# Performance work log

Hardware: AMD Instinct MI355X
Metric: run time of the kernel (lower is better)

The kernel has to match this reference:

```python
import jax, jax.numpy as jnp
import numpy as np

B, NE, DE = 4096, 64, 96
NA, NACT = 8, 16
DH, NH, OD = 256, 4, 64
HD = DH // NH


def setup_inputs() -> dict:
    key = jax.random.key(0)
    ks = jax.random.split(key, 16)
    s = 0.02
    entities = jax.random.normal(ks[0], (B, NE, DE), jnp.float32)
    entity_mask = jax.random.randint(ks[1], (B, NE), 0, 2, jnp.int32)
    obs_mask = jax.random.randint(ks[2], (B, NE, NE), 0, 2, jnp.int32)
    act_ids = jax.random.randint(ks[3], (B, NA), 0, NACT)
    actions_onehot = jax.nn.one_hot(act_ids, NACT, dtype=jnp.float32)
    return {
        "entities": entities,
        "entity_mask": entity_mask,
        "obs_mask": obs_mask,
        "actions_onehot": actions_onehot,
        "We": jax.random.normal(ks[4], (DE, DH), jnp.float32) * s,
        "be": jnp.zeros((DH,), jnp.float32),
        "Wa": jax.random.normal(ks[5], (NACT, DH), jnp.float32) * s,
        "Win": jax.random.normal(ks[6], (DH, 3 * DH), jnp.float32) * s,
        "Wout": jax.random.normal(ks[7], (DH, DH), jnp.float32) * s,
        "bout": jnp.zeros((DH,), jnp.float32),
        "Wm1": jax.random.normal(ks[8], (DH, DH), jnp.float32) * s,
        "bm1": jnp.zeros((DH,), jnp.float32),
        "Wm2": jax.random.normal(ks[9], (DH, OD), jnp.float32) * s,
        "bm2": jnp.zeros((OD,), jnp.float32),
        "Wl1": jax.random.normal(ks[10], (DH, DH), jnp.float32) * s,
        "bl1": jnp.zeros((DH,), jnp.float32),
        "Wl2": jax.random.normal(ks[11], (DH, OD), jnp.float32) * s,
        "bl2": jnp.zeros((OD,), jnp.float32),
    }


def reference(entities, entity_mask, obs_mask, actions_onehot,
              We, be, Wa, Win, Wout, bout,
              Wm1, bm1, Wm2, bm2, Wl1, bl1, Wl2, bl2):
    # entity encode + action embed, scattered into first NA entity slots
    he = entities @ We + be                      # [B, NE, DH]
    ha = actions_onehot @ Wa                     # [B, NA, DH]
    ha_pad = jnp.zeros_like(he).at[:, :NA].set(ha)
    x = jax.nn.relu(he + ha_pad)                 # [B, NE, DH]

    # multi-head attention: NA agent queries attend to NE entities
    qkv = x @ Win                                # [B, NE, 3*DH]
    q, k, v = jnp.split(qkv, 3, axis=-1)
    q = q[:, :NA].reshape(B, NA, NH, HD)
    k = k.reshape(B, NE, NH, HD)
    v = v.reshape(B, NE, NH, HD)
    logits = jnp.einsum('bqhd,bkhd->bhqk', q, k) / jnp.sqrt(jnp.float32(HD))
    pre = obs_mask[:, :NA, :NE].astype(bool)[:, None, :, :]  # [B,1,NA,NE]
    logits = jnp.where(pre, -jnp.inf, logits)
    w = jax.nn.softmax(logits, axis=-1)
    w = jnp.where(jnp.isnan(w), 0.0, w)          # fully-masked rows -> 0
    attn = jnp.einsum('bhqk,bkhd->bqhd', w, v).reshape(B, NA, DH)
    attn = attn @ Wout + bout
    post = entity_mask[:, :NA].astype(bool)[..., None]  # [B, NA, 1]
    hidden = jax.nn.relu(jnp.where(post, 0.0, attn))

    mean = jax.nn.relu(hidden @ Wm1 + bm1) @ Wm2 + bm2
    logvar = jnp.clip(jax.nn.relu(hidden @ Wl1 + bl1) @ Wl2 + bl2, -10.0, 0.0)
    return mean, logvar
```

## Files before the change

kernel.cpp:

```cpp
#include <hip/hip_runtime.h>
#include <hip/hip_bf16.h>
#include <math.h>

typedef __attribute__((ext_vector_type(8))) short short8;
typedef __attribute__((ext_vector_type(4))) float f32x4;

#define DEVINL static __device__ __forceinline__

static constexpr int NBPB = 2;
static constexpr int NBLK = 4096 / NBPB;

static constexpr int WE_OFF  = 0;
static constexpr int WQ_OFF  = 24576;
static constexpr int WK_OFF  = 90112;
static constexpr int WV_OFF  = 155648;
static constexpr int WO_OFF  = 221184;
static constexpr int WM1_OFF = 286720;
static constexpr int WM2_OFF = 352256;
static constexpr int WL1_OFF = 368640;
static constexpr int WL2_OFF = 434176;

static constexpr int XOFF    = 0;
static constexpr int KOFF    = 65536;
static constexpr int VOFF    = 65536;
static constexpr int HID_OFF = 65536;
static constexpr int M1_OFF  = 81920;
static constexpr int L1_OFF  = 98304;
static constexpr int QOFF    = 131072;
static constexpr int WOFF2   = 147456;
static constexpr int EOFF    = 131072;
static constexpr int ACT_OFF = 155648;
static constexpr int LDS_BYTES = 155712;

DEVINL unsigned short f2bf(float f) {
  union { float f; unsigned u; } x; x.f = f;
  unsigned r = x.u + 0x7fffu + ((x.u >> 16) & 1u);
  return (unsigned short)(r >> 16);
}

DEVINL f32x4 mfma(short8 a, short8 b, f32x4 c) {
  return __builtin_amdgcn_mfma_f32_16x16x32_bf16(a, b, c, 0, 0, 0);
}

DEVINL short8 ldfrag(const unsigned short* wf, int off, int nt, int kt, int nkt, int lane) {
  return *(const short8*)(wf + off + ((nt * nkt + kt) << 9) + (lane << 3));
}

DEVINL short8 lda512(const char* sm, int base, int row, int colbyte) {
  return *(const short8*)(sm + base + row * 512 + (colbyte ^ ((row & 7) << 4)));
}

DEVINL void stb512(char* sm, int base, int row, int col, float v) {
  *(unsigned short*)(sm + base + row * 512 + ((col * 2) ^ ((row & 7) << 4))) = f2bf(v);
}

__global__ __launch_bounds__(512) void prep_kernel(
    const float* We, const float* Win, const float* Wout, const float* Wm1,
    const float* Wm2, const float* Wl1, const float* Wl2, unsigned short* wf) {
  const int m = blockIdx.y;
  const int Ks[9]   = {96, 256, 256, 256, 256, 256, 256, 256, 256};
  const int Ns[9]   = {256, 256, 256, 256, 256, 256, 64, 256, 64};
  const int lds_[9] = {256, 768, 768, 768, 256, 256, 64, 256, 64};
  const int coff[9] = {0, 0, 256, 512, 0, 0, 0, 0, 0};
  const int dsto[9] = {WE_OFF, WQ_OFF, WK_OFF, WV_OFF, WO_OFF, WM1_OFF, WM2_OFF, WL1_OFF, WL2_OFF};
  const float* srcs[9] = {We, Win, Win, Win, Wout, Wm1, Wm2, Wl1, Wl2};
  const int K = Ks[m], N = Ns[m], nkt = K / 32;
  const int total = (N / 16) * nkt * 512;
  const int idx = blockIdx.x * 512 + threadIdx.x;
  if (idx >= total) return;
  const int j = idx & 7, lane = (idx >> 3) & 63;
  const int kt = (idx >> 9) % nkt, nt = idx / (512 * nkt);
  const int row = kt * 32 + ((lane >> 4) << 3) + j;
  const int col = nt * 16 + (lane & 15);
  wf[dsto[m] + idx] = f2bf(srcs[m][(long)row * lds_[m] + coff[m] + col]);
}

__global__ __launch_bounds__(512, 2) void fused_kernel(
    const float* __restrict__ entities, const int* __restrict__ entity_mask,
    const int* __restrict__ obs_mask, const float* __restrict__ acts,
    const float* __restrict__ Wa, const float* __restrict__ be,
    const float* __restrict__ bout, const float* __restrict__ bm1,
    const float* __restrict__ bm2, const float* __restrict__ bl1,
    const float* __restrict__ bl2, const unsigned short* __restrict__ wf,
    float* __restrict__ out) {
  extern __shared__ char sm[];
  const int tid = threadIdx.x;
  const int w = tid >> 6, lane = tid & 63;
  const int g = lane >> 4, c = lane & 15;
  const int ig0 = blockIdx.x * 2;
  const int nt0 = w * 2;

  {
    const int it = tid >> 8, i = tid & 255;
    const int row = i >> 2, q4 = i & 3;
    const float* src = entities + (long)(ig0 + it) * 6144 + row * 96 + q4 * 24;
    const int ebase = EOFF + it * 12288 + row * 192;
    const int sw = (row & 3) << 4;
#pragma unroll
    for (int ch = 0; ch < 3; ++ch) {
      short8 s;
#pragma unroll
      for (int k = 0; k < 8; ++k) s[k] = (short)f2bf(src[ch * 8 + k]);
      *(short8*)(sm + ebase + ((q4 * 48 + ch * 16) ^ sw)) = s;
    }
    if (tid < 16) {
      const float* oh = acts + ((long)(ig0 + (tid >> 3)) * 8 + (tid & 7)) * 16;
      int id = 0;
      for (int a = 0; a < 16; ++a) if (oh[a] > 0.5f) id = a;
      ((int*)(sm + ACT_OFF))[tid] = id;
    }
  }
  __syncthreads();

  {
    f32x4 acc[2][4][2] = {};
#pragma unroll
    for (int kt = 0; kt < 3; ++kt) {
      short8 b0 = ldfrag(wf, WE_OFF, nt0, kt, 3, lane);
      short8 b1 = ldfrag(wf, WE_OFF, nt0 + 1, kt, 3, lane);
#pragma unroll
      for (int it = 0; it < 2; ++it)
#pragma unroll
        for (int mt = 0; mt < 4; ++mt) {
          const int row = mt * 16 + c;
          short8 a = *(const short8*)(sm + EOFF + it * 12288 + row * 192 +
                                      ((kt * 64 + (g << 4)) ^ ((row & 3) << 4)));
          acc[it][mt][0] = mfma(a, b0, acc[it][mt][0]);
          acc[it][mt][1] = mfma(a, b1, acc[it][mt][1]);
        }
    }
    float bev[2] = {be[nt0 * 16 + c], be[nt0 * 16 + 16 + c]};
#pragma unroll
    for (int it = 0; it < 2; ++it)
#pragma unroll
      for (int mt = 0; mt < 4; ++mt)
#pragma unroll
        for (int n = 0; n < 2; ++n)
#pragma unroll
          for (int r = 0; r < 4; ++r) {
            const int row = mt * 16 + g * 4 + r;
            const int col = (nt0 + n) * 16 + c;
            float v = acc[it][mt][n][r] + bev[n];
            if (row < 8) {
              int id = ((const int*)(sm + ACT_OFF))[it * 8 + row];
              v += Wa[id * 256 + col];
            }
            v = fmaxf(v, 0.f);
            stb512(sm, XOFF + it * 32768, row, col, v);
          }
  }
  __syncthreads();

  {
    f32x4 qa[2][2] = {};
#pragma unroll
    for (int kt = 0; kt < 8; ++kt) {
      short8 b0 = ldfrag(wf, WQ_OFF, nt0, kt, 8, lane);
      short8 b1 = ldfrag(wf, WQ_OFF, nt0 + 1, kt, 8, lane);
#pragma unroll
      for (int it = 0; it < 2; ++it) {
        short8 a = lda512(sm, XOFF + it * 32768, c, kt * 64 + (g << 4));
        qa[it][0] = mfma(a, b0, qa[it][0]);
        qa[it][1] = mfma(a, b1, qa[it][1]);
      }
    }
#pragma unroll
    for (int it = 0; it < 2; ++it)
#pragma unroll
      for (int n = 0; n < 2; ++n)
#pragma unroll
        for (int r = 0; r < 4; ++r)
          stb512(sm, QOFF + it * 8192, g * 4 + r, (nt0 + n) * 16 + c, qa[it][n][r]);
  }
  __syncthreads();

  {
    f32x4 acc[2][4][2] = {};
#pragma unroll
    for (int kt = 0; kt < 8; ++kt) {
      short8 b0 = ldfrag(wf, WK_OFF, nt0, kt, 8, lane);
      short8 b1 = ldfrag(wf, WK_OFF, nt0 + 1, kt, 8, lane);
#pragma unroll
      for (int it = 0; it < 2; ++it)
#pragma unroll
        for (int mt = 0; mt < 4; ++mt) {
          short8 a = lda512(sm, XOFF + it * 32768, mt * 16 + c, kt * 64 + (g << 4));
          acc[it][mt][0] = mfma(a, b0, acc[it][mt][0]);
          acc[it][mt][1] = mfma(a, b1, acc[it][mt][1]);
        }
    }
#pragma unroll
    for (int it = 0; it < 2; ++it)
#pragma unroll
      for (int mt = 0; mt < 4; ++mt)
#pragma unroll
        for (int n = 0; n < 2; ++n)
#pragma unroll
          for (int r = 0; r < 4; ++r)
            stb512(sm, KOFF + it * 32768, mt * 16 + g * 4 + r, (nt0 + n) * 16 + c,
                   acc[it][mt][n][r]);
  }
  __syncthreads();

  {
    const int it = w >> 2, h = w & 3;
    const long ig = ig0 + it;
    f32x4 lac[4] = {};
#pragma unroll
    for (int kt = 0; kt < 2; ++kt) {
      const int colb = h * 128 + kt * 64 + (g << 4);
      short8 aq = lda512(sm, QOFF + it * 8192, c, colb);
#pragma unroll
      for (int nt = 0; nt < 4; ++nt) {
        short8 bk = lda512(sm, KOFF + it * 32768, nt * 16 + c, colb);
        lac[nt] = mfma(aq, bk, lac[nt]);
      }
    }
    const int* obs = obs_mask + ig * 4096;
#pragma unroll
    for (int r = 0; r < 4; ++r) {
      const int qi = g * 4 + r;
      float vals[4];
#pragma unroll
      for (int nt = 0; nt < 4; ++nt) {
        int msk = obs[qi * 64 + nt * 16 + c];
        vals[nt] = msk ? -INFINITY : lac[nt][r] * 0.125f;
      }
      float mx = fmaxf(fmaxf(vals[0], vals[1]), fmaxf(vals[2], vals[3]));
#pragma unroll
      for (int d = 1; d < 16; d <<= 1) mx = fmaxf(mx, __shfl_xor(mx, d, 64));
      float s = 0.f;
#pragma unroll
      for (int nt = 0; nt < 4; ++nt) {
        float e = (mx == -INFINITY) ? 0.f : expf(vals[nt] - mx);
        vals[nt] = e; s += e;
      }
#pragma unroll
      for (int d = 1; d < 16; d <<= 1) s += __shfl_xor(s, d, 64);
      const float inv = (s > 0.f) ? 1.f / s : 0.f;
      if (qi < 8) {
#pragma unroll
        for (int nt = 0; nt < 4; ++nt) {
          const int key = nt * 16 + c;
          *(unsigned short*)(sm + WOFF2 + ((it * 4 + h) * 8 + qi) * 128 +
                             ((key * 2) ^ (qi << 4))) = f2bf(vals[nt] * inv);
        }
      }
    }
  }
  __syncthreads();

  {
    f32x4 acc[2][4][2] = {};
#pragma unroll
    for (int kt = 0; kt < 8; ++kt) {
      short8 b0 = ldfrag(wf, WV_OFF, nt0, kt, 8, lane);
      short8 b1 = ldfrag(wf, WV_OFF, nt0 + 1, kt, 8, lane);
#pragma unroll
      for (int it = 0; it < 2; ++it)
#pragma unroll
        for (int mt = 0; mt < 4; ++mt) {
          short8 a = lda512(sm, XOFF + it * 32768, mt * 16 + c, kt * 64 + (g << 4));
          acc[it][mt][0] = mfma(a, b0, acc[it][mt][0]);
          acc[it][mt][1] = mfma(a, b1, acc[it][mt][1]);
        }
    }
#pragma unroll
    for (int it = 0; it < 2; ++it)
#pragma unroll
      for (int mt = 0; mt < 4; ++mt)
#pragma unroll
        for (int n = 0; n < 2; ++n) {
          const int d = (nt0 + n) * 16 + c;
          const int key0 = mt * 16 + g * 4;
          unsigned long long pk = 0;
#pragma unroll
          for (int r = 0; r < 4; ++r)
            pk |= (unsigned long long)f2bf(acc[it][mt][n][r]) << (16 * r);
          *(unsigned long long*)(sm + VOFF + it * 32768 + d * 128 +
                                 ((key0 * 2) ^ ((d & 7) << 4))) = pk;
        }
  }
  __syncthreads();

  {
    const int it = w >> 2, h = w & 3;
    f32x4 aac[4] = {};
#pragma unroll
    for (int kt = 0; kt < 2; ++kt) {
      const int kb = kt * 64 + (g << 4);
      const int wrow = c & 7;
      short8 aw = *(const short8*)(sm + WOFF2 + ((it * 4 + h) * 8 + wrow) * 128 +
                                   (kb ^ (wrow << 4)));
#pragma unroll
      for (int n = 0; n < 4; ++n) {
        const int d = (h * 4 + n) * 16 + c;
        short8 bv = *(const short8*)(sm + VOFF + it * 32768 + d * 128 +
                                     (kb ^ ((d & 7) << 4)));
        aac[n] = mfma(aw, bv, aac[n]);
      }
    }
#pragma unroll
    for (int n = 0; n < 4; ++n)
#pragma unroll
      for (int r = 0; r < 4; ++r)
        stb512(sm, QOFF + it * 8192, g * 4 + r, (h * 4 + n) * 16 + c, aac[n][r]);
  }
  __syncthreads();

  {
    f32x4 acc[2][2] = {};
#pragma unroll
    for (int kt = 0; kt < 8; ++kt) {
      short8 b0 = ldfrag(wf, WO_OFF, nt0, kt, 8, lane);
      short8 b1 = ldfrag(wf, WO_OFF, nt0 + 1, kt, 8, lane);
#pragma unroll
      for (int it = 0; it < 2; ++it) {
        short8 a = lda512(sm, QOFF + it * 8192, c, kt * 64 + (g << 4));
        acc[it][0] = mfma(a, b0, acc[it][0]);
        acc[it][1] = mfma(a, b1, acc[it][1]);
      }
    }
    float bo[2] = {bout[nt0 * 16 + c], bout[nt0 * 16 + 16 + c]};
#pragma unroll
    for (int it = 0; it < 2; ++it) {
      const int* em = entity_mask + (long)(ig0 + it) * 64;
#pragma unroll
      for (int n = 0; n < 2; ++n)
#pragma unroll
        for (int r = 0; r < 4; ++r) {
          const int row = g * 4 + r;
          float v = acc[it][n][r] + bo[n];
          v = em[row] ? 0.f : fmaxf(v, 0.f);
          stb512(sm, HID_OFF + it * 8192, row, (nt0 + n) * 16 + c, v);
        }
    }
  }
  __syncthreads();

  {
    f32x4 am[2][2] = {}, al[2][2] = {};
#pragma unroll
    for (int kt = 0; kt < 8; ++kt) {
      short8 bm0 = ldfrag(wf, WM1_OFF, nt0, kt, 8, lane);
      short8 bm1f = ldfrag(wf, WM1_OFF, nt0 + 1, kt, 8, lane);
      short8 bl0 = ldfrag(wf, WL1_OFF, nt0, kt, 8, lane);
      short8 bl1f = ldfrag(wf, WL1_OFF, nt0 + 1, kt, 8, lane);
#pragma unroll
      for (int it = 0; it < 2; ++it) {
        short8 a = lda512(sm, HID_OFF + it * 8192, c, kt * 64 + (g << 4));
        am[it][0] = mfma(a, bm0, am[it][0]);
        am[it][1] = mfma(a, bm1f, am[it][1]);
        al[it][0] = mfma(a, bl0, al[it][0]);
        al[it][1] = mfma(a, bl1f, al[it][1]);
      }
    }
    float bmv[2] = {bm1[nt0 * 16 + c], bm1[nt0 * 16 + 16 + c]};
    float blv[2] = {bl1[nt0 * 16 + c], bl1[nt0 * 16 + 16 + c]};
#pragma unroll
    for (int it = 0; it < 2; ++it)
#pragma unroll
      for (int n = 0; n < 2; ++n)
#pragma unroll
        for (int r = 0; r < 4; ++r) {
          const int row = g * 4 + r, col = (nt0 + n) * 16 + c;
          stb512(sm, M1_OFF + it * 8192, row, col, fmaxf(am[it][n][r] + bmv[n], 0.f));
          stb512(sm, L1_OFF + it * 8192, row, col, fmaxf(al[it][n][r] + blv[n], 0.f));
        }
  }
  __syncthreads();

  {
    const int isv = (w >= 4);
    const int nt = w & 3;
    const int SRC = (isv ? L1_OFF : M1_OFF);
    const int WOF = (isv ? WL2_OFF : WM2_OFF);
    const float* bias = isv ? bl2 : bm2;
    f32x4 acc[2] = {};
#pragma unroll
    for (int kt = 0; kt < 8; ++kt) {
      short8 b = ldfrag(wf, WOF, nt, kt, 8, lane);
#pragma unroll
      for (int it = 0; it < 2; ++it) {
        short8 a = lda512(sm, SRC + it * 8192, c, kt * 64 + (g << 4));
        acc[it] = mfma(a, b, acc[it]);
      }
    }
    const float bv = bias[nt * 16 + c];
    const long obase = isv ? 2097152L : 0L;
#pragma unroll
    for (int it = 0; it < 2; ++it)
#pragma unroll
      for (int r = 0; r < 4; ++r) {
        const int qi = g * 4 + r;
        if (qi < 8) {
          float v = acc[it][r] + bv;
          if (isv) v = fminf(fmaxf(v, -10.f), 0.f);
          out[obase + (long)(ig0 + it) * 512 + qi * 64 + nt * 16 + c] = v;
        }
      }
  }
}

extern "C" void kernel_launch(void* const* d_in, const int* in_sizes, int n_in,
                              void* d_out, int out_size, void* d_ws, size_t ws_size,
                              hipStream_t stream) {
  const float* entities   = (const float*)d_in[0];
  const int*   entity_mask= (const int*)d_in[1];
  const int*   obs_mask   = (const int*)d_in[2];
  const float* acts       = (const float*)d_in[3];
  const float* We   = (const float*)d_in[4];
  const float* be   = (const float*)d_in[5];
  const float* Wa   = (const float*)d_in[6];
  const float* Win  = (const float*)d_in[7];
  const float* Wout = (const float*)d_in[8];
  const float* bout = (const float*)d_in[9];
  const float* Wm1  = (const float*)d_in[10];
  const float* bm1  = (const float*)d_in[11];
  const float* Wm2  = (const float*)d_in[12];
  const float* bm2  = (const float*)d_in[13];
  const float* Wl1  = (const float*)d_in[14];
  const float* bl1  = (const float*)d_in[15];
  const float* Wl2  = (const float*)d_in[16];
  const float* bl2  = (const float*)d_in[17];
  unsigned short* wf = (unsigned short*)d_ws;

  prep_kernel<<<dim3(128, 9), 512, 0, stream>>>(We, Win, Wout, Wm1, Wm2, Wl1, Wl2, wf);

  hipFuncSetAttribute((const void*)fused_kernel,
                      hipFuncAttributeMaxDynamicSharedMemorySize, LDS_BYTES);
  fused_kernel<<<NBLK, 512, LDS_BYTES, stream>>>(
      entities, entity_mask, obs_mask, acts, Wa, be, bout, bm1, bm2, bl1, bl2,
      wf, (float*)d_out);
}
```

Before: 419.5 us.

## Reassociate attention to skip full K and V projections, use 1024 threads

The attention is rewritten algebraically. Queries are multiplied by the transposed per-head Wk, so logits are computed directly against x and the full K projection is never formed. The softmax weights are applied to x before projecting through Wv, so only 16 query rows are projected instead of 64 entity rows. The block grows to 1024 threads (16 waves) with a new LDS layout that also keeps a transposed copy of x. Entity loading is vectorized, and the prep kernel is rewritten, with a special transposed layout for Wk. Extra barriers and more LDS (164KB) may limit occupancy to one block per CU.

```diff
diff --git a/kernel.cpp b/kernel.cpp
--- a/kernel.cpp
+++ b/kernel.cpp
@@ -4,15 +4,15 @@
 
 typedef __attribute__((ext_vector_type(8))) short short8;
 typedef __attribute__((ext_vector_type(4))) float f32x4;
+typedef __attribute__((ext_vector_type(2))) unsigned int uint2v;
 
 #define DEVINL static __device__ __forceinline__
 
-static constexpr int NBPB = 2;
-static constexpr int NBLK = 4096 / NBPB;
+static constexpr int NBLK = 2048;
 
 static constexpr int WE_OFF  = 0;
 static constexpr int WQ_OFF  = 24576;
-static constexpr int WK_OFF  = 90112;
+static constexpr int WKT_OFF = 90112;
 static constexpr int WV_OFF  = 155648;
 static constexpr int WO_OFF  = 221184;
 static constexpr int WM1_OFF = 286720;
@@ -20,17 +20,19 @@
 static constexpr int WL1_OFF = 368640;
 static constexpr int WL2_OFF = 434176;
 
-static constexpr int XOFF    = 0;
-static constexpr int KOFF    = 65536;
-static constexpr int VOFF    = 65536;
-static constexpr int HID_OFF = 65536;
-static constexpr int M1_OFF  = 81920;
-static constexpr int L1_OFF  = 98304;
-static constexpr int QOFF    = 131072;
-static constexpr int WOFF2   = 147456;
-static constexpr int EOFF    = 131072;
-static constexpr int ACT_OFF = 155648;
-static constexpr int LDS_BYTES = 155712;
+static constexpr int XOFF   = 0;
+static constexpr int WLOFF  = 0;
+static constexpr int ATOFF  = 8192;
+static constexpr int HOFF   = 16384;
+static constexpr int M1OFF  = 24576;
+static constexpr int L1OFF  = 32768;
+static constexpr int XTOFF  = 65536;
+static constexpr int EOFF   = 131072;
+static constexpr int TOFF   = 131072;
+static constexpr int WXOFF  = 131072;
+static constexpr int ACTOFF = 155648;
+static constexpr int QOFF   = 155648;
+static constexpr int LDS_BYTES = 163840;
 
 DEVINL unsigned short f2bf(float f) {
   union { float f; unsigned u; } x; x.f = f;
@@ -46,36 +48,36 @@
   return *(const short8*)(wf + off + ((nt * nkt + kt) << 9) + (lane << 3));
 }
 
-DEVINL short8 lda512(const char* sm, int base, int row, int colbyte) {
-  return *(const short8*)(sm + base + row * 512 + (colbyte ^ ((row & 7) << 4)));
-}
-
-DEVINL void stb512(char* sm, int base, int row, int col, float v) {
-  *(unsigned short*)(sm + base + row * 512 + ((col * 2) ^ ((row & 7) << 4))) = f2bf(v);
-}
-
 __global__ __launch_bounds__(512) void prep_kernel(
     const float* We, const float* Win, const float* Wout, const float* Wm1,
     const float* Wm2, const float* Wl1, const float* Wl2, unsigned short* wf) {
   const int m = blockIdx.y;
-  const int Ks[9]   = {96, 256, 256, 256, 256, 256, 256, 256, 256};
-  const int Ns[9]   = {256, 256, 256, 256, 256, 256, 64, 256, 64};
-  const int lds_[9] = {256, 768, 768, 768, 256, 256, 64, 256, 64};
-  const int coff[9] = {0, 0, 256, 512, 0, 0, 0, 0, 0};
-  const int dsto[9] = {WE_OFF, WQ_OFF, WK_OFF, WV_OFF, WO_OFF, WM1_OFF, WM2_OFF, WL1_OFF, WL2_OFF};
-  const float* srcs[9] = {We, Win, Win, Win, Wout, Wm1, Wm2, Wl1, Wl2};
-  const int K = Ks[m], N = Ns[m], nkt = K / 32;
-  const int total = (N / 16) * nkt * 512;
   const int idx = blockIdx.x * 512 + threadIdx.x;
-  if (idx >= total) return;
-  const int j = idx & 7, lane = (idx >> 3) & 63;
-  const int kt = (idx >> 9) % nkt, nt = idx / (512 * nkt);
-  const int row = kt * 32 + ((lane >> 4) << 3) + j;
-  const int col = nt * 16 + (lane & 15);
-  wf[dsto[m] + idx] = f2bf(srcs[m][(long)row * lds_[m] + coff[m] + col]);
-}
-
-__global__ __launch_bounds__(512, 2) void fused_kernel(
+  if (m == 2) {
+    if (idx >= 65536) return;
+    const int h = idx >> 14, d = (idx >> 6) & 255, hd = idx & 63;
+    const float v = Win[(long)d * 768 + 256 + h * 64 + hd];
+    const int kt = hd >> 5, gg = (hd >> 3) & 3, j = hd & 7;
+    wf[WKT_OFF + (((h * 16 + (d >> 4)) * 2 + kt) << 9) + (gg * 16 + (d & 15)) * 8 + j] =
+        f2bf(v);
+    return;
+  }
+  const int Ks[9]  = {96, 256, 0, 256, 256, 256, 256, 256, 256};
+  const int Ns[9]  = {256, 256, 0, 256, 256, 256, 64, 256, 64};
+  const int ld_[9] = {256, 768, 0, 768, 256, 256, 64, 256, 64};
+  const int co_[9] = {0, 0, 0, 512, 0, 0, 0, 0, 0};
+  const int off[9] = {WE_OFF, WQ_OFF, 0, WV_OFF, WO_OFF, WM1_OFF, WM2_OFF, WL1_OFF, WL2_OFF};
+  const float* S[9] = {We, Win, Win, Win, Wout, Wm1, Wm2, Wl1, Wl2};
+  const int K = Ks[m], N = Ns[m];
+  if (idx >= K * N) return;
+  const int row = idx / N, col = idx - row * N;
+  const float v = S[m][(long)row * ld_[m] + co_[m] + col];
+  const int nkt = K >> 5;
+  wf[off[m] + ((((col >> 4) * nkt) + (row >> 5)) << 9) +
+     ((((row >> 3) & 3) << 4) + (col & 15)) * 8 + (row & 7)] = f2bf(v);
+}
+
+__global__ __launch_bounds__(1024, 4) void fused_kernel(
     const float* __restrict__ entities, const int* __restrict__ entity_mask,
     const int* __restrict__ obs_mask, const float* __restrict__ acts,
     const float* __restrict__ Wa, const float* __restrict__ be,
@@ -88,327 +90,312 @@
   const int w = tid >> 6, lane = tid & 63;
   const int g = lane >> 4, c = lane & 15;
   const int ig0 = blockIdx.x * 2;
-  const int nt0 = w * 2;
-
-  {
-    const int it = tid >> 8, i = tid & 255;
-    const int row = i >> 2, q4 = i & 3;
-    const float* src = entities + (long)(ig0 + it) * 6144 + row * 96 + q4 * 24;
+
+  {
+    const int it = tid >> 9, i = tid & 511;
+    const int row = i >> 3, seg = i & 7;
+    const float* src = entities + (long)(ig0 + it) * 6144 + row * 96 + seg * 12;
     const int ebase = EOFF + it * 12288 + row * 192;
     const int sw = (row & 3) << 4;
 #pragma unroll
-    for (int ch = 0; ch < 3; ++ch) {
-      short8 s;
-#pragma unroll
-      for (int k = 0; k < 8; ++k) s[k] = (short)f2bf(src[ch * 8 + k]);
-      *(short8*)(sm + ebase + ((q4 * 48 + ch * 16) ^ sw)) = s;
+    for (int p = 0; p < 3; ++p) {
+      float4 f = *(const float4*)(src + p * 4);
+      uint2v u;
+      u.x = f2bf(f.x) | ((unsigned)f2bf(f.y) << 16);
+      u.y = f2bf(f.z) | ((unsigned)f2bf(f.w) << 16);
+      *(uint2v*)(sm + ebase + ((seg * 24 + p * 8) ^ sw)) = u;
     }
     if (tid < 16) {
       const float* oh = acts + ((long)(ig0 + (tid >> 3)) * 8 + (tid & 7)) * 16;
       int id = 0;
+#pragma unroll
       for (int a = 0; a < 16; ++a) if (oh[a] > 0.5f) id = a;
-      ((int*)(sm + ACT_OFF))[tid] = id;
-    }
-  }
-  __syncthreads();
-
-  {
-    f32x4 acc[2][4][2] = {};
+      ((int*)(sm + ACTOFF))[tid] = id;
+    }
+  }
+  __syncthreads();
+
+  {
+    f32x4 acc[2][4] = {};
 #pragma unroll
     for (int kt = 0; kt < 3; ++kt) {
-      short8 b0 = ldfrag(wf, WE_OFF, nt0, kt, 3, lane);
-      short8 b1 = ldfrag(wf, WE_OFF, nt0 + 1, kt, 3, lane);
+      short8 b = ldfrag(wf, WE_OFF, w, kt, 3, lane);
 #pragma unroll
       for (int it = 0; it < 2; ++it)
 #pragma unroll
         for (int mt = 0; mt < 4; ++mt) {
           const int row = mt * 16 + c;
           short8 a = *(const short8*)(sm + EOFF + it * 12288 + row * 192 +
-                                      ((kt * 64 + (g << 4)) ^ ((row & 3) << 4)));
-          acc[it][mt][0] = mfma(a, b0, acc[it][mt][0]);
-          acc[it][mt][1] = mfma(a, b1, acc[it][mt][1]);
-        }
-    }
-    float bev[2] = {be[nt0 * 16 + c], be[nt0 * 16 + 16 + c]};
+                                      ((kt * 64 + g * 16) ^ ((row & 3) << 4)));
+          acc[it][mt] = mfma(a, b, acc[it][mt]);
+        }
+    }
+    const int col = w * 16 + c;
+    const float bev = be[col];
 #pragma unroll
     for (int it = 0; it < 2; ++it)
 #pragma unroll
-      for (int mt = 0; mt < 4; ++mt)
-#pragma unroll
-        for (int n = 0; n < 2; ++n)
-#pragma unroll
-          for (int r = 0; r < 4; ++r) {
-            const int row = mt * 16 + g * 4 + r;
-            const int col = (nt0 + n) * 16 + c;
-            float v = acc[it][mt][n][r] + bev[n];
-            if (row < 8) {
-              int id = ((const int*)(sm + ACT_OFF))[it * 8 + row];
-              v += Wa[id * 256 + col];
-            }
-            v = fmaxf(v, 0.f);
-            stb512(sm, XOFF + it * 32768, row, col, v);
+      for (int mt = 0; mt < 4; ++mt) {
+        float vv[4];
+#pragma unroll
+        for (int r = 0; r < 4; ++r) {
+          const int row = mt * 16 + g * 4 + r;
+          float v = acc[it][mt][r] + bev;
+          if (row < 8) {
+            int id = ((const int*)(sm + ACTOFF))[it * 8 + row];
+            v += Wa[id * 256 + col];
           }
-  }
-  __syncthreads();
-
-  {
-    f32x4 qa[2][2] = {};
+          v = fmaxf(v, 0.f);
+          vv[r] = v;
+          *(unsigned short*)(sm + XOFF + it * 32768 + row * 512 +
+                             ((col * 2) ^ ((row & 7) << 4))) = f2bf(v);
+        }
+        uint2v u;
+        u.x = f2bf(vv[0]) | ((unsigned)f2bf(vv[1]) << 16);
+        u.y = f2bf(vv[2]) | ((unsigned)f2bf(vv[3]) << 16);
+        *(uint2v*)(sm + XTOFF + it * 32768 + col * 128 +
+                   ((mt * 32 + g * 8) ^ ((col & 7) << 4))) = u;
+      }
+  }
+  __syncthreads();
+
+  {
+    f32x4 qa = {0.f, 0.f, 0.f, 0.f};
 #pragma unroll
     for (int kt = 0; kt < 8; ++kt) {
-      short8 b0 = ldfrag(wf, WQ_OFF, nt0, kt, 8, lane);
-      short8 b1 = ldfrag(wf, WQ_OFF, nt0 + 1, kt, 8, lane);
-#pragma unroll
-      for (int it = 0; it < 2; ++it) {
-        short8 a = lda512(sm, XOFF + it * 32768, c, kt * 64 + (g << 4));
-        qa[it][0] = mfma(a, b0, qa[it][0]);
-        qa[it][1] = mfma(a, b1, qa[it][1]);
-      }
-    }
-#pragma unroll
-    for (int it = 0; it < 2; ++it)
-#pragma unroll
-      for (int n = 0; n < 2; ++n)
-#pragma unroll
-        for (int r = 0; r < 4; ++r)
-          stb512(sm, QOFF + it * 8192, g * 4 + r, (nt0 + n) * 16 + c, qa[it][n][r]);
-  }
-  __syncthreads();
-
-  {
-    f32x4 acc[2][4][2] = {};
-#pragma unroll
-    for (int kt = 0; kt < 8; ++kt) {
-      short8 b0 = ldfrag(wf, WK_OFF, nt0, kt, 8, lane);
-      short8 b1 = ldfrag(wf, WK_OFF, nt0 + 1, kt, 8, lane);
-#pragma unroll
-      for (int it = 0; it < 2; ++it)
-#pragma unroll
-        for (int mt = 0; mt < 4; ++mt) {
-          short8 a = lda512(sm, XOFF + it * 32768, mt * 16 + c, kt * 64 + (g << 4));
-          acc[it][mt][0] = mfma(a, b0, acc[it][mt][0]);
-          acc[it][mt][1] = mfma(a, b1, acc[it][mt][1]);
-        }
-    }
-#pragma unroll
-    for (int it = 0; it < 2; ++it)
-#pragma unroll
-      for (int mt = 0; mt < 4; ++mt)
-#pragma unroll
-        for (int n = 0; n < 2; ++n)
-#pragma unroll
-          for (int r = 0; r < 4; ++r)
-            stb512(sm, KOFF + it * 32768, mt * 16 + g * 4 + r, (nt0 + n) * 16 + c,
-                   acc[it][mt][n][r]);
-  }
-  __syncthreads();
-
-  {
-    const int it = w >> 2, h = w & 3;
-    const long ig = ig0 + it;
+      short8 b = ldfrag(wf, WQ_OFF, w, kt, 8, lane);
+      short8 a = *(const short8*)(sm + XOFF + (c >> 3) * 32768 + (c & 7) * 512 +
+                                  ((kt * 64 + g * 16) ^ ((c & 7) << 4)));
+      qa = mfma(a, b, qa);
+    }
+#pragma unroll
+    for (int r = 0; r < 4; ++r) {
+      const int qq = g * 4 + r;
+      *(unsigned short*)(sm + QOFF + qq * 512 +
+                         (((w * 16 + c) * 2) ^ ((qq & 7) << 4))) = f2bf(qa[r]);
+    }
+  }
+  __syncthreads();
+
+  {
+    const int h = w >> 2, dq = w & 3;
+    f32x4 ta[4] = {};
+#pragma unroll
+    for (int kt = 0; kt < 2; ++kt) {
+      short8 a = *(const short8*)(sm + QOFF + c * 512 +
+                                  ((h * 128 + kt * 64 + g * 16) ^ ((c & 7) << 4)));
+#pragma unroll
+      for (int n = 0; n < 4; ++n) {
+        short8 b = ldfrag(wf, WKT_OFF, h * 16 + dq * 4 + n, kt, 2, lane);
+        ta[n] = mfma(a, b, ta[n]);
+      }
+    }
+    __syncthreads();
+#pragma unroll
+    for (int n = 0; n < 4; ++n)
+#pragma unroll
+      for (int r = 0; r < 4; ++r) {
+        const int qq = g * 4 + r;
+        const int col = (dq * 4 + n) * 16 + c;
+        *(unsigned short*)(sm + TOFF + h * 8192 + qq * 512 +
+                           ((col * 2) ^ ((qq & 7) << 4))) = f2bf(ta[n][r]);
+      }
+  }
+  __syncthreads();
+
+  {
+    const int it = (w >> 2) & 1, h = w & 3;
+    float wvals[4][4];
     f32x4 lac[4] = {};
-#pragma unroll
-    for (int kt = 0; kt < 2; ++kt) {
-      const int colb = h * 128 + kt * 64 + (g << 4);
-      short8 aq = lda512(sm, QOFF + it * 8192, c, colb);
-#pragma unroll
-      for (int nt = 0; nt < 4; ++nt) {
-        short8 bk = lda512(sm, KOFF + it * 32768, nt * 16 + c, colb);
-        lac[nt] = mfma(aq, bk, lac[nt]);
-      }
-    }
-    const int* obs = obs_mask + ig * 4096;
-#pragma unroll
-    for (int r = 0; r < 4; ++r) {
-      const int qi = g * 4 + r;
-      float vals[4];
-#pragma unroll
-      for (int nt = 0; nt < 4; ++nt) {
-        int msk = obs[qi * 64 + nt * 16 + c];
-        vals[nt] = msk ? -INFINITY : lac[nt][r] * 0.125f;
-      }
-      float mx = fmaxf(fmaxf(vals[0], vals[1]), fmaxf(vals[2], vals[3]));
-#pragma unroll
-      for (int d = 1; d < 16; d <<= 1) mx = fmaxf(mx, __shfl_xor(mx, d, 64));
-      float s = 0.f;
-#pragma unroll
-      for (int nt = 0; nt < 4; ++nt) {
-        float e = (mx == -INFINITY) ? 0.f : expf(vals[nt] - mx);
-        vals[nt] = e; s += e;
-      }
-#pragma unroll
-      for (int d = 1; d < 16; d <<= 1) s += __shfl_xor(s, d, 64);
-      const float inv = (s > 0.f) ? 1.f / s : 0.f;
-      if (qi < 8) {
+    if (w < 8) {
+#pragma unroll
+      for (int kt = 0; kt < 8; ++kt) {
+        short8 a = *(const short8*)(sm + TOFF + h * 8192 + (it * 8 + (c & 7)) * 512 +
+                                    ((kt * 64 + g * 16) ^ ((c & 7) << 4)));
 #pragma unroll
         for (int nt = 0; nt < 4; ++nt) {
           const int key = nt * 16 + c;
-          *(unsigned short*)(sm + WOFF2 + ((it * 4 + h) * 8 + qi) * 128 +
-                             ((key * 2) ^ (qi << 4))) = f2bf(vals[nt] * inv);
-        }
-      }
-    }
-  }
-  __syncthreads();
-
-  {
-    f32x4 acc[2][4][2] = {};
-#pragma unroll
-    for (int kt = 0; kt < 8; ++kt) {
-      short8 b0 = ldfrag(wf, WV_OFF, nt0, kt, 8, lane);
-      short8 b1 = ldfrag(wf, WV_OFF, nt0 + 1, kt, 8, lane);
-#pragma unroll
-      for (int it = 0; it < 2; ++it)
-#pragma unroll
-        for (int mt = 0; mt < 4; ++mt) {
-          short8 a = lda512(sm, XOFF + it * 32768, mt * 16 + c, kt * 64 + (g << 4));
-          acc[it][mt][0] = mfma(a, b0, acc[it][mt][0]);
-          acc[it][mt][1] = mfma(a, b1, acc[it][mt][1]);
-        }
-    }
-#pragma unroll
-    for (int it = 0; it < 2; ++it)
-#pragma unroll
-      for (int mt = 0; mt < 4; ++mt)
-#pragma unroll
-        for (int n = 0; n < 2; ++n) {
-          const int d = (nt0 + n) * 16 + c;
-          const int key0 = mt * 16 + g * 4;
-          unsigned long long pk = 0;
-#pragma unroll
-          for (int r = 0; r < 4; ++r)
-            pk |= (unsigned long long)f2bf(acc[it][mt][n][r]) << (16 * r);
-          *(unsigned long long*)(sm + VOFF + it * 32768 + d * 128 +
-                                 ((key0 * 2) ^ ((d & 7) << 4))) = pk;
-        }
-  }
-  __syncthreads();
-
-  {
-    const int it = w >> 2, h = w & 3;
-    f32x4 aac[4] = {};
-#pragma unroll
-    for (int kt = 0; kt < 2; ++kt) {
-      const int kb = kt * 64 + (g << 4);
-      const int wrow = c & 7;
-      short8 aw = *(const short8*)(sm + WOFF2 + ((it * 4 + h) * 8 + wrow) * 128 +
-                                   (kb ^ (wrow << 4)));
-#pragma unroll
-      for (int n = 0; n < 4; ++n) {
-        const int d = (h * 4 + n) * 16 + c;
-        short8 bv = *(const short8*)(sm + VOFF + it * 32768 + d * 128 +
-                                     (kb ^ ((d & 7) << 4)));
-        aac[n] = mfma(aw, bv, aac[n]);
-      }
-    }
-#pragma unroll
-    for (int n = 0; n < 4; ++n)
-#pragma unroll
-      for (int r = 0; r < 4; ++r)
-        stb512(sm, QOFF + it * 8192, g * 4 + r, (h * 4 + n) * 16 + c, aac[n][r]);
-  }
-  __syncthreads();
-
-  {
-    f32x4 acc[2][2] = {};
-#pragma unroll
-    for (int kt = 0; kt < 8; ++kt) {
-      short8 b0 = ldfrag(wf, WO_OFF, nt0, kt, 8, lane);
-      short8 b1 = ldfrag(wf, WO_OFF, nt0 + 1, kt, 8, lane);
-#pragma unroll
-      for (int it = 0; it < 2; ++it) {
-        short8 a = lda512(sm, QOFF + it * 8192, c, kt * 64 + (g << 4));
-        acc[it][0] = mfma(a, b0, acc[it][0]);
-        acc[it][1] = mfma(a, b1, acc[it][1]);
-      }
-    }
-    float bo[2] = {bout[nt0 * 16 + c], bout[nt0 * 16 + 16 + c]};
-#pragma unroll
-    for (int it = 0; it < 2; ++it) {
-      const int* em = entity_mask + (long)(ig0 + it) * 64;
-#pragma unroll
-      for (int n = 0; n < 2; ++n)
+          short8 b = *(const short8*)(sm + XOFF + it * 32768 + key * 512 +
+                                      ((kt * 64 + g * 16) ^ ((key & 7) << 4)));
+          lac[nt] = mfma(a, b, lac[nt]);
+        }
+      }
+      if (g < 2) {
+        const int* obs = obs_mask + (long)(ig0 + it) * 4096;
 #pragma unroll
         for (int r = 0; r < 4; ++r) {
-          const int row = g * 4 + r;
-          float v = acc[it][n][r] + bo[n];
-          v = em[row] ? 0.f : fmaxf(v, 0.f);
-          stb512(sm, HID_OFF + it * 8192, row, (nt0 + n) * 16 + c, v);
-        }
-    }
-  }
-  __syncthreads();
-
-  {
-    f32x4 am[2][2] = {}, al[2][2] = {};
-#pragma unroll
-    for (int kt = 0; kt < 8; ++kt) {
-      short8 bm0 = ldfrag(wf, WM1_OFF, nt0, kt, 8, lane);
-      short8 bm1f = ldfrag(wf, WM1_OFF, nt0 + 1, kt, 8, lane);
-      short8 bl0 = ldfrag(wf, WL1_OFF, nt0, kt, 8, lane);
-      short8 bl1f = ldfrag(wf, WL1_OFF, nt0 + 1, kt, 8, lane);
-#pragma unroll
-      for (int it = 0; it < 2; ++it) {
-        short8 a = lda512(sm, HID_OFF + it * 8192, c, kt * 64 + (g << 4));
-        am[it][0] = mfma(a, bm0, am[it][0]);
-        am[it][1] = mfma(a, bm1f, am[it][1]);
-        al[it][0] = mfma(a, bl0, al[it][0]);
-        al[it][1] = mfma(a, bl1f, al[it][1]);
-      }
-    }
-    float bmv[2] = {bm1[nt0 * 16 + c], bm1[nt0 * 16 + 16 + c]};
-    float blv[2] = {bl1[nt0 * 16 + c], bl1[nt0 * 16 + 16 + c]};
-#pragma unroll
-    for (int it = 0; it < 2; ++it)
-#pragma unroll
-      for (int n = 0; n < 2; ++n)
-#pragma unroll
-        for (int r = 0; r < 4; ++r) {
-          const int row = g * 4 + r, col = (nt0 + n) * 16 + c;
-          stb512(sm, M1_OFF + it * 8192, row, col, fmaxf(am[it][n][r] + bmv[n], 0.f));
-          stb512(sm, L1_OFF + it * 8192, row, col, fmaxf(al[it][n][r] + blv[n], 0.f));
-        }
-  }
-  __syncthreads();
-
-  {
-    const int isv = (w >= 4);
-    const int nt = w & 3;
-    const int SRC = (isv ? L1_OFF : M1_OFF);
-    const int WOF = (isv ? WL2_OFF : WM2_OFF);
-    const float* bias = isv ? bl2 : bm2;
-    f32x4 acc[2] = {};
-#pragma unroll
-    for (int kt = 0; kt < 8; ++kt) {
-      short8 b = ldfrag(wf, WOF, nt, kt, 8, lane);
-#pragma unroll
-      for (int it = 0; it < 2; ++it) {
-        short8 a = lda512(sm, SRC + it * 8192, c, kt * 64 + (g << 4));
-        acc[it] = mfma(a, b, acc[it]);
-      }
-    }
-    const float bv = bias[nt * 16 + c];
-    const long obase = isv ? 2097152L : 0L;
-#pragma unroll
-    for (int it = 0; it < 2; ++it)
+          const int qi = g * 4 + r;
+          float vals[4];
+#pragma unroll
+          for (int nt = 0; nt < 4; ++nt) {
+            int msk = obs[qi * 64 + nt * 16 + c];
+            vals[nt] = msk ? -INFINITY : lac[nt][r] * 0.125f;
+          }
+          float mx = fmaxf(fmaxf(vals[0], vals[1]), fmaxf(vals[2], vals[3]));
+#pragma unroll
+          for (int d = 1; d < 16; d <<= 1) mx = fmaxf(mx, __shfl_xor(mx, d, 64));
+          float s = 0.f;
+#pragma unroll
+          for (int nt = 0; nt < 4; ++nt) {
+            float e = (mx == -INFINITY) ? 0.f : expf(vals[nt] - mx);
+            vals[nt] = e; s += e;
+          }
+#pragma unroll
+          for (int d = 1; d < 16; d <<= 1) s += __shfl_xor(s, d, 64);
+          const float inv = (s > 0.f) ? 1.f / s : 0.f;
+#pragma unroll
+          for (int nt = 0; nt < 4; ++nt) wvals[r][nt] = vals[nt] * inv;
+        }
+      }
+    }
+    __syncthreads();
+    if (w < 8 && g < 2) {
 #pragma unroll
       for (int r = 0; r < 4; ++r) {
         const int qi = g * 4 + r;
-        if (qi < 8) {
-          float v = acc[it][r] + bv;
-          if (isv) v = fminf(fmaxf(v, -10.f), 0.f);
-          out[obase + (long)(ig0 + it) * 512 + qi * 64 + nt * 16 + c] = v;
-        }
-      }
+#pragma unroll
+        for (int nt = 0; nt < 4; ++nt) {
+          const int key = nt * 16 + c;
+          *(unsigned short*)(sm + WLOFF + ((it * 4 + h) * 8 + qi) * 128 +
+                             ((key * 2) ^ ((qi & 7) << 4))) = f2bf(wvals[r][nt]);
+        }
+      }
+    }
+  }
+  __syncthreads();
+
+  {
+    const int it = w >> 3, h = (w >> 1) & 3, dh = w & 1;
+    f32x4 xa[8] = {};
+#pragma unroll
+    for (int kt = 0; kt < 2; ++kt) {
+      short8 a = *(const short8*)(sm + WLOFF + ((it * 4 + h) * 8 + (c & 7)) * 128 +
+                                  ((kt * 64 + g * 16) ^ ((c & 7) << 4)));
+#pragma unroll
+      for (int n = 0; n < 8; ++n) {
+        const int d = dh * 128 + n * 16 + c;
+        short8 b = *(const short8*)(sm + XTOFF + it * 32768 + d * 128 +
+                                    ((kt * 64 + g * 16) ^ ((d & 7) << 4)));
+        xa[n] = mfma(a, b, xa[n]);
+      }
+    }
+    if (g < 2) {
+#pragma unroll
+      for (int n = 0; n < 8; ++n)
+#pragma unroll
+        for (int r = 0; r < 4; ++r) {
+          const int qq = it * 8 + g * 4 + r;
+          const int col = h * 256 + dh * 128 + n * 16 + c;
+          *(unsigned short*)(sm + WXOFF + qq * 2048 +
+                             ((col * 2) ^ ((qq & 7) << 4))) = f2bf(xa[n][r]);
+        }
+    }
+  }
+  __syncthreads();
+
+  {
+    const int h = w >> 2, n = w & 3;
+    f32x4 aac = {0.f, 0.f, 0.f, 0.f};
+#pragma unroll
+    for (int kt = 0; kt < 8; ++kt) {
+      short8 a = *(const short8*)(sm + WXOFF + c * 2048 +
+                                  ((h * 512 + kt * 64 + g * 16) ^ ((c & 7) << 4)));
+      short8 b = ldfrag(wf, WV_OFF, h * 4 + n, kt, 8, lane);
+      aac = mfma(a, b, aac);
+    }
+#pragma unroll
+    for (int r = 0; r < 4; ++r) {
+      const int qq = g * 4 + r;
+      const int col = (h * 4 + n) * 16 + c;
+      *(unsigned short*)(sm + ATOFF + qq * 512 +
+                         ((col * 2) ^ ((qq & 7) << 4))) = f2bf(aac[r]);
+    }
+  }
+  __syncthreads();
+
+  {
+    f32x4 hc = {0.f, 0.f, 0.f, 0.f};
+#pragma unroll
+    for (int kt = 0; kt < 8; ++kt) {
+      short8 a = *(const short8*)(sm + ATOFF + c * 512 +
+                                  ((kt * 64 + g * 16) ^ ((c & 7) << 4)));
+      short8 b = ldfrag(wf, WO_OFF, w, kt, 8, lane);
+      hc = mfma(a, b, hc);
+    }
+    const int col = w * 16 + c;
+    const float bo = bout[col];
+#pragma unroll
+    for (int r = 0; r < 4; ++r) {
+      const int qq = g * 4 + r;
+      const int em = entity_mask[(long)(ig0 + (qq >> 3)) * 64 + (qq & 7)];
+      float v = hc[r] + bo;
+      v = em ? 0.f : fmaxf(v, 0.f);
+      *(unsigned short*)(sm + HOFF + qq * 512 + ((col * 2) ^ ((qq & 7) << 4))) = f2bf(v);
+    }
+  }
+  __syncthreads();
+
+  {
+    const int which = w >> 3, np = w & 7;
+    const int woff = which ? WL1_OFF : WM1_OFF;
+    const float* bias = which ? bl1 : bm1;
+    const int base = which ? L1OFF : M1OFF;
+    f32x4 mc[2] = {};
+#pragma unroll
+    for (int kt = 0; kt < 8; ++kt) {
+      short8 a = *(const short8*)(sm + HOFF + c * 512 +
+                                  ((kt * 64 + g * 16) ^ ((c & 7) << 4)));
+      short8 b0 = ldfrag(wf, woff, np * 2, kt, 8, lane);
+      short8 b1 = ldfrag(wf, woff, np * 2 + 1, kt, 8, lane);
+      mc[0] = mfma(a, b0, mc[0]);
+      mc[1] = mfma(a, b1, mc[1]);
+    }
+#pragma unroll
+    for (int n = 0; n < 2; ++n) {
+      const int col = (np * 2 + n) * 16 + c;
+      const float bv = bias[col];
+#pragma unroll
+      for (int r = 0; r < 4; ++r) {
+        const int qq = g * 4 + r;
+        float v = fmaxf(mc[n][r] + bv, 0.f);
+        *(unsigned short*)(sm + base + qq * 512 + ((col * 2) ^ ((qq & 7) << 4))) = f2bf(v);
+      }
+    }
+  }
+  __syncthreads();
+
+  if (w < 8) {
+    const int which = w >> 2, nt = w & 3;
+    const int woff = which ? WL2_OFF : WM2_OFF;
+    const int base = which ? L1OFF : M1OFF;
+    const float* bias = which ? bl2 : bm2;
+    f32x4 oc = {0.f, 0.f, 0.f, 0.f};
+#pragma unroll
+    for (int kt = 0; kt < 8; ++kt) {
+      short8 a = *(const short8*)(sm + base + c * 512 +
+                                  ((kt * 64 + g * 16) ^ ((c & 7) << 4)));
+      short8 b = ldfrag(wf, woff, nt, kt, 8, lane);
+      oc = mfma(a, b, oc);
+    }
+    const float bv = bias[nt * 16 + c];
+#pragma unroll
+    for (int r = 0; r < 4; ++r) {
+      const int qq = g * 4 + r;
+      float v = oc[r] + bv;
+      if (which) v = fminf(fmaxf(v, -10.f), 0.f);
+      out[(long)which * 2097152 + (long)(ig0 + (qq >> 3)) * 512 + (qq & 7) * 64 +
+          nt * 16 + c] = v;
+    }
   }
 }
 
 extern "C" void kernel_launch(void* const* d_in, const int* in_sizes, int n_in,
                               void* d_out, int out_size, void* d_ws, size_t ws_size,
                               hipStream_t stream) {
-  const float* entities   = (const float*)d_in[0];
-  const int*   entity_mask= (const int*)d_in[1];
-  const int*   obs_mask   = (const int*)d_in[2];
-  const float* acts       = (const float*)d_in[3];
+  const float* entities    = (const float*)d_in[0];
+  const int*   entity_mask = (const int*)d_in[1];
+  const int*   obs_mask    = (const int*)d_in[2];
+  const float* acts        = (const float*)d_in[3];
   const float* We   = (const float*)d_in[4];
   const float* be   = (const float*)d_in[5];
   const float* Wa   = (const float*)d_in[6];
@@ -429,7 +416,7 @@
 
   hipFuncSetAttribute((const void*)fused_kernel,
                       hipFuncAttributeMaxDynamicSharedMemorySize, LDS_BYTES);
-  fused_kernel<<<NBLK, 512, LDS_BYTES, stream>>>(
+  fused_kernel<<<NBLK, 1024, LDS_BYTES, stream>>>(
       entities, entity_mask, obs_mask, acts, Wa, be, bout, bm1, bm2, bl1, bl2,
       wf, (float*)d_out);
 }
```

Result: faster. 352.6 us (-15.9%).
